# Optimization experiments

Hardware: AMD Instinct MI355X
Metric: run time of the kernel (lower is better)

Reference implementation:

```python
import jax, jax.numpy as jnp
import numpy as np

MARGIN = 0.1  # GatingFunction margin_threshold default


def _gating(x, gW1, gb1, gW2, gb2):
    # two-layer MLP + softmax over experts: [B, E]
    h = jax.nn.relu(x @ gW1 + gb1)
    probs = jax.nn.softmax(h @ gW2 + gb2, axis=1)

    # sequential per-sample running-assignment masking (training + mask_enabled path)
    def step(rta, s):
        rta1 = rta + s
        mask = rta1 > rta1.mean() + MARGIN
        rta2 = jnp.where(mask.any(), rta1 - s, rta1)  # subtract back only if any masked
        mod = jnp.where(mask, 0.0, s)
        norm = mod.sum()
        mod = mod / jnp.where(norm == 0, 1.0, norm)
        return rta2 + mod, mod

    rta0 = jnp.zeros((gW2.shape[1],), probs.dtype)  # running_total_assignment buffer
    _, gate = jax.lax.scan(step, rta0, probs)
    # torch code writes detached modified samples into modified_x -> no grad through gate
    return jax.lax.stop_gradient(gate)


def reference(x_expert, gW1, gb1, gW2, gb2, eW1, eb1, eW2, eb2):
    gate = _gating(x_expert, gW1, gb1, gW2, gb2)          # [B, E]
    # all experts run densely: [B, E, H] -> [B, E, O]
    h = jax.nn.relu(jnp.einsum('bi,eih->beh', x_expert, eW1) + eb1)
    expert_out = jnp.einsum('beh,eho->beo', h, eW2) + eb2
    g = gate[:, :, None]                                   # [B, E, 1]
    # fallback if every gate value is zero (torch's all-zero check)
    g = jnp.where(jnp.all(g == 0), jnp.ones_like(g) / g.shape[1], g)
    output = jnp.sum(g * expert_out, axis=1)               # [B, O]
    return output, g


def setup_inputs() -> dict:
    B, IN, HID, OUT, E = 4096, 1024, 4096, 1024, 8
    key = jax.random.key(0)
    ks = jax.random.split(key, 9)
    s = 0.02
    return {
        'x_expert': jax.random.normal(ks[0], (B, IN), jnp.float32),
        'gW1': jax.random.normal(ks[1], (IN, HID), jnp.float32) * s,
        'gb1': jnp.zeros((HID,), jnp.float32),
        'gW2': jax.random.normal(ks[2], (HID, E), jnp.float32) * s,
        'gb2': jnp.zeros((E,), jnp.float32),
        'eW1': jax.random.normal(ks[3], (E, IN, HID), jnp.float32) * s,
        'eb1': jnp.zeros((E, HID), jnp.float32),
        'eW2': jax.random.normal(ks[4], (E, HID, OUT), jnp.float32) * s,
        'eb2': jnp.zeros((E, OUT), jnp.float32),
    }
```

## Files before the change

### kernel.cpp

```cpp
#include <hip/hip_runtime.h>
#include <stdint.h>

using f32x4  = __attribute__((ext_vector_type(4))) float;
using bf16x8 = __attribute__((ext_vector_type(8))) __bf16;

static __device__ __forceinline__ unsigned int f2bf_u(float f) {
  union { float f; unsigned int u; } v; v.f = f;
  return (v.u + 0x7fffu + ((v.u >> 16) & 1u)) >> 16;
}
static __device__ __forceinline__ unsigned short f2bf(float f) {
  return (unsigned short)f2bf_u(f);
}

static __device__ __forceinline__ void gload_lds16(const void* g, void* l) {
  __builtin_amdgcn_global_load_lds((const __attribute__((address_space(1))) void*)g,
                                   (__attribute__((address_space(3))) void*)l,
                                   16, 0, 0);
}

static __device__ __forceinline__ int swz(int row) { return (row & 3) ^ ((row >> 2) & 3); }

template <int CTRL>
static __device__ __forceinline__ float dppadd(float x) {
  int xi = __builtin_bit_cast(int, x);
  int yi = __builtin_amdgcn_update_dpp(0, xi, CTRL, 0xF, 0xF, true);
  return x + __builtin_bit_cast(float, yi);
}
static __device__ __forceinline__ float redsum8(float x) {
  float t = dppadd<0xB1>(x);
  t = dppadd<0x4E>(t);
  t = dppadd<0x124>(t);
  return t;
}

__global__ __launch_bounds__(256) void k_cvt_bf16(const float* __restrict__ in,
                                                  unsigned short* __restrict__ out) {
  int i = blockIdx.x * 256 + threadIdx.x;
  float4 v = ((const float4*)in)[i];
  ushort4 o;
  o.x = f2bf(v.x); o.y = f2bf(v.y); o.z = f2bf(v.z); o.w = f2bf(v.w);
  ((ushort4*)out)[i] = o;
}

__global__ __launch_bounds__(256) void k_transpose_cvt(const float* __restrict__ in,
                                                       unsigned short* __restrict__ out,
                                                       int R, int C) {
  __shared__ float tile[32][33];
  int e = blockIdx.z;
  const float* ip = in + (size_t)e * R * C;
  unsigned short* op = out + (size_t)e * R * C;
  int c0 = blockIdx.x * 32, r0 = blockIdx.y * 32;
  int tx = threadIdx.x, ty = threadIdx.y;
  #pragma unroll
  for (int i = ty; i < 32; i += 8)
    tile[i][tx] = ip[(size_t)(r0 + i) * C + c0 + tx];
  __syncthreads();
  #pragma unroll
  for (int i = ty; i < 32; i += 8)
    op[(size_t)(c0 + i) * R + r0 + tx] = f2bf(tile[tx][i]);
}

__global__ __launch_bounds__(256, 2) void k_gemm_f32_relu(const float* __restrict__ A,
                                                          const float* __restrict__ Bm,
                                                          const float* __restrict__ bias,
                                                          float* __restrict__ C) {
  const int K = 1024, N = 4096;
  __shared__ float As[16][256];
  __shared__ float Bs[16][128];
  int n0 = blockIdx.x * 128, m0 = blockIdx.y * 256;
  int t = threadIdx.x;
  int tm = t >> 4, tn = t & 15;
  float acc[16][8];
  #pragma unroll
  for (int i = 0; i < 16; ++i)
    #pragma unroll
    for (int j = 0; j < 8; ++j) acc[i][j] = 0.f;

  for (int k0 = 0; k0 < K; k0 += 16) {
    __syncthreads();
    #pragma unroll
    for (int cc = 0; cc < 4; ++cc) {
      int c = t + cc * 256;
      int m = c >> 2, kq = c & 3;
      float4 v = *(const float4*)&A[(size_t)(m0 + m) * K + k0 + kq * 4];
      As[kq * 4 + 0][m] = v.x; As[kq * 4 + 1][m] = v.y;
      As[kq * 4 + 2][m] = v.z; As[kq * 4 + 3][m] = v.w;
    }
    #pragma unroll
    for (int cc = 0; cc < 2; ++cc) {
      int c = t + cc * 256;
      int kr = c >> 5, nq = c & 31;
      *(float4*)&Bs[kr][nq * 4] = *(const float4*)&Bm[(size_t)(k0 + kr) * N + n0 + nq * 4];
    }
    __syncthreads();
    #pragma unroll
    for (int kk = 0; kk < 16; ++kk) {
      float a[16], b[8];
      #pragma unroll
      for (int q = 0; q < 4; ++q)
        *(float4*)&a[q * 4] = *(const float4*)&As[kk][tm * 16 + q * 4];
      *(float4*)&b[0] = *(const float4*)&Bs[kk][tn * 8];
      *(float4*)&b[4] = *(const float4*)&Bs[kk][tn * 8 + 4];
      #pragma unroll
      for (int i = 0; i < 16; ++i)
        #pragma unroll
        for (int j = 0; j < 8; ++j) acc[i][j] = fmaf(a[i], b[j], acc[i][j]);
    }
  }
  float bb[8];
  #pragma unroll
  for (int j = 0; j < 8; ++j) bb[j] = bias[n0 + tn * 8 + j];
  #pragma unroll
  for (int i = 0; i < 16; ++i) {
    int m = m0 + tm * 16 + i;
    float* crow = C + (size_t)m * N + n0 + tn * 8;
    float4 v0, v1;
    v0.x = fmaxf(acc[i][0] + bb[0], 0.f); v0.y = fmaxf(acc[i][1] + bb[1], 0.f);
    v0.z = fmaxf(acc[i][2] + bb[2], 0.f); v0.w = fmaxf(acc[i][3] + bb[3], 0.f);
    v1.x = fmaxf(acc[i][4] + bb[4], 0.f); v1.y = fmaxf(acc[i][5] + bb[5], 0.f);
    v1.z = fmaxf(acc[i][6] + bb[6], 0.f); v1.w = fmaxf(acc[i][7] + bb[7], 0.f);
    *(float4*)crow = v0; *(float4*)(crow + 4) = v1;
  }
}

__global__ __launch_bounds__(256) void k_gate2_softmax(const float* __restrict__ Hg,
                                                       const float* __restrict__ gW2,
                                                       const float* __restrict__ gb2,
                                                       float* __restrict__ probs) {
  __shared__ float red[4][8];
  int b = blockIdx.x, t = threadIdx.x;
  const float* hrow = Hg + (size_t)b * 4096;
  float acc[8];
  #pragma unroll
  for (int e = 0; e < 8; ++e) acc[e] = 0.f;
  #pragma unroll
  for (int i = 0; i < 4; ++i) {
    int kk = t + i * 256;
    float4 h = ((const float4*)hrow)[kk];
    const float* wr = gW2 + (size_t)kk * 32;
    #pragma unroll
    for (int j = 0; j < 4; ++j) {
      float hv = (&h.x)[j];
      #pragma unroll
      for (int e = 0; e < 8; ++e) acc[e] = fmaf(hv, wr[j * 8 + e], acc[e]);
    }
  }
  #pragma unroll
  for (int e = 0; e < 8; ++e) {
    float v = acc[e];
    for (int off = 32; off > 0; off >>= 1) v += __shfl_down(v, off);
    acc[e] = v;
  }
  int lane = t & 63, w = t >> 6;
  if (lane == 0) {
    #pragma unroll
    for (int e = 0; e < 8; ++e) red[w][e] = acc[e];
  }
  __syncthreads();
  if (t == 0) {
    float l[8], mx = -1e30f;
    #pragma unroll
    for (int e = 0; e < 8; ++e) {
      l[e] = red[0][e] + red[1][e] + red[2][e] + red[3][e] + gb2[e];
      mx = fmaxf(mx, l[e]);
    }
    float sum = 0.f;
    #pragma unroll
    for (int e = 0; e < 8; ++e) { l[e] = expf(l[e] - mx); sum += l[e]; }
    float inv = 1.f / sum;
    #pragma unroll
    for (int e = 0; e < 8; ++e) probs[b * 8 + e] = l[e] * inv;
  }
}

__global__ __launch_bounds__(256) void k_egemm1_scan(const unsigned short* __restrict__ Xb,
                                                     const unsigned short* __restrict__ W1T,
                                                     const float* __restrict__ eb1,
                                                     const float* __restrict__ probs,
                                                     float* __restrict__ gateOut,
                                                     unsigned short* __restrict__ Hs) {
  __shared__ __align__(16) char smem[16512];
  int bid = blockIdx.x;
  int t = threadIdx.x;

  if (bid == 0) {
    float* P  = (float*)smem;
    float* G  = P + 2048;
    int*  flg = (int*)(G + 2048);
    int e = t & 7;
    float rta = 0.f, maxn = 0.f;
    for (int ch = 0; ch < 16; ++ch) {
      __syncthreads();
      #pragma unroll
      for (int i = 0; i < 2; ++i)
        ((float4*)P)[t + i * 256] = ((const float4*)(probs + ch * 2048))[t + i * 256];
      __syncthreads();
      if (t < 64) {
        float s_cur = P[e];
        for (int r = 0; r < 256; ++r) {
          float s_nxt = P[(((r + 1) & 255) << 3) + e];
          float a = rta + s_cur;
          float sum = redsum8(a);
          float thr = fmaf(sum, 0.125f, 0.1f);
          bool msk = a > thr;
          unsigned long long bal = __ballot(msk);
          float d = msk ? 0.f : s_cur;
          float norm = redsum8(d);
          float inv = (norm == 0.f) ? 1.f : (1.f / norm);
          float g = d * inv;
          float base = (bal != 0ull) ? (a - s_cur) : a;
          rta = base + g;
          maxn = fmaxf(maxn, norm);
          if (t < 8) G[(r << 3) + e] = g;
          s_cur = s_nxt;
        }
      }
      __syncthreads();
      #pragma unroll
      for (int i = 0; i < 2; ++i)
        ((float4*)(gateOut + ch * 2048))[t + i * 256] = ((const float4*)G)[t + i * 256];
    }
    if (t == 0) *flg = (maxn > 0.f) ? 1 : 0;
    __syncthreads();
    if (*flg == 0) {
      for (int i = t; i < 32768; i += 256) gateOut[i] = 0.125f;
    }
    return;
  }

  char* Asm = smem;
  char* Bsm = smem + 8192;
  int b = bid - 1;
  int e = b >> 10;
  int rest = b & 1023;
  int m0 = (rest >> 5) << 7, n0 = (rest & 31) << 7;
  int lane = t & 63, w = t >> 6;
  int wm = w >> 1, wn = w & 1;
  const unsigned short* Ab = Xb;
  const unsigned short* Bb = W1T + ((size_t)e << 22);
  f32x4 acc[4][4];
  #pragma unroll
  for (int mi = 0; mi < 4; ++mi)
    #pragma unroll
    for (int ni = 0; ni < 4; ++ni) acc[mi][ni] = (f32x4){0.f, 0.f, 0.f, 0.f};

  for (int kt = 0; kt < 1024; kt += 32) {
    __syncthreads();
    {
      int p = (w << 6) + lane;
      int row = p >> 2, h = (p & 3) ^ swz(row);
      int p2 = p + 256;
      int row2 = p2 >> 2, h2 = (p2 & 3) ^ swz(row2);
      char* la = Asm + (w << 10);
      char* lb = Bsm + (w << 10);
      gload_lds16(Ab + (size_t)(m0 + row) * 1024 + kt + h * 8, la);
      gload_lds16(Ab + (size_t)(m0 + row2) * 1024 + kt + h2 * 8, la + 4096);
      gload_lds16(Bb + (size_t)(n0 + row) * 1024 + kt + h * 8, lb);
      gload_lds16(Bb + (size_t)(n0 + row2) * 1024 + kt + h2 * 8, lb + 4096);
    }
    __syncthreads();
    bf16x8 af[4], bfr[4];
    #pragma unroll
    for (int mi = 0; mi < 4; ++mi) {
      int ra = (wm << 6) + (mi << 4) + (lane & 15);
      int hh = (lane >> 4) ^ swz(ra);
      af[mi] = *(const bf16x8*)(Asm + ra * 64 + hh * 16);
    }
    #pragma unroll
    for (int ni = 0; ni < 4; ++ni) {
      int rb = (wn << 6) + (ni << 4) + (lane & 15);
      int hh = (lane >> 4) ^ swz(rb);
      bfr[ni] = *(const bf16x8*)(Bsm + rb * 64 + hh * 16);
    }
    #pragma unroll
    for (int mi = 0; mi < 4; ++mi)
      #pragma unroll
      for (int ni = 0; ni < 4; ++ni)
        acc[mi][ni] = __builtin_amdgcn_mfma_f32_16x16x32_bf16(bfr[ni], af[mi], acc[mi][ni], 0, 0, 0);
  }
  const float* b1e = eb1 + (e << 12);
  unsigned short* Ho = Hs + ((size_t)e << 24);
  int col = lane & 15, quad = lane >> 4;
  float4 bq[4];
  #pragma unroll
  for (int ni = 0; ni < 4; ++ni)
    bq[ni] = *(const float4*)&b1e[n0 + (wn << 6) + (ni << 4) + (quad << 2)];
  #pragma unroll
  for (int mi = 0; mi < 4; ++mi) {
    int m = m0 + (wm << 6) + (mi << 4) + col;
    unsigned short* orow = Ho + (size_t)m * 4096 + n0 + (wn << 6) + (quad << 2);
    #pragma unroll
    for (int ni = 0; ni < 4; ++ni) {
      float v0 = fmaxf(acc[mi][ni][0] + bq[ni].x, 0.f);
      float v1 = fmaxf(acc[mi][ni][1] + bq[ni].y, 0.f);
      float v2 = fmaxf(acc[mi][ni][2] + bq[ni].z, 0.f);
      float v3 = fmaxf(acc[mi][ni][3] + bq[ni].w, 0.f);
      uint2 u;
      u.x = f2bf_u(v0) | (f2bf_u(v1) << 16);
      u.y = f2bf_u(v2) | (f2bf_u(v3) << 16);
      *(uint2*)(orow + (ni << 4)) = u;
    }
  }
}

__global__ __launch_bounds__(256) void k_egemm2(const unsigned short* __restrict__ Hs,
                                                const unsigned short* __restrict__ W2T,
                                                float* __restrict__ partLo,
                                                float* __restrict__ partHi) {
  __shared__ __align__(16) char Asm[8192];
  __shared__ __align__(16) char Bsm[8192];
  int bid = blockIdx.x;
  int n0 = (bid >> 8) << 7;
  int rem = bid & 255;
  int m0 = (rem >> 3) << 7;
  int e = rem & 7;
  int t = threadIdx.x, lane = t & 63, w = t >> 6;
  int wm = w >> 1, wn = w & 1;
  const unsigned short* Ab = Hs + ((size_t)e << 24);
  const unsigned short* Bb = W2T + ((size_t)e << 22);
  f32x4 acc[4][4];
  #pragma unroll
  for (int mi = 0; mi < 4; ++mi)
    #pragma unroll
    for (int ni = 0; ni < 4; ++ni) acc[mi][ni] = (f32x4){0.f, 0.f, 0.f, 0.f};

  for (int kt = 0; kt < 4096; kt += 32) {
    __syncthreads();
    {
      int p = (w << 6) + lane;
      int row = p >> 2, h = (p & 3) ^ swz(row);
      int p2 = p + 256;
      int row2 = p2 >> 2, h2 = (p2 & 3) ^ swz(row2);
      char* la = Asm + (w << 10);
      char* lb = Bsm + (w << 10);
      gload_lds16(Ab + (size_t)(m0 + row) * 4096 + kt + h * 8, la);
      gload_lds16(Ab + (size_t)(m0 + row2) * 4096 + kt + h2 * 8, la + 4096);
      gload_lds16(Bb + (size_t)(n0 + row) * 4096 + kt + h * 8, lb);
      gload_lds16(Bb + (size_t)(n0 + row2) * 4096 + kt + h2 * 8, lb + 4096);
    }
    __syncthreads();
    bf16x8 af[4], bfr[4];
    #pragma unroll
    for (int mi = 0; mi < 4; ++mi) {
      int ra = (wm << 6) + (mi << 4) + (lane & 15);
      int hh = (lane >> 4) ^ swz(ra);
      af[mi] = *(const bf16x8*)(Asm + ra * 64 + hh * 16);
    }
    #pragma unroll
    for (int ni = 0; ni < 4; ++ni) {
      int rb = (wn << 6) + (ni << 4) + (lane & 15);
      int hh = (lane >> 4) ^ swz(rb);
      bfr[ni] = *(const bf16x8*)(Bsm + rb * 64 + hh * 16);
    }
    #pragma unroll
    for (int mi = 0; mi < 4; ++mi)
      #pragma unroll
      for (int ni = 0; ni < 4; ++ni)
        acc[mi][ni] = __builtin_amdgcn_mfma_f32_16x16x32_bf16(bfr[ni], af[mi], acc[mi][ni], 0, 0, 0);
  }
  float* Pe = (e < 4 ? partLo + ((size_t)e << 22) : partHi + ((size_t)(e - 4) << 22));
  int col = lane & 15, quad = lane >> 4;
  #pragma unroll
  for (int mi = 0; mi < 4; ++mi) {
    int m = m0 + (wm << 6) + (mi << 4) + col;
    float* orow = Pe + (size_t)m * 1024 + n0 + (wn << 6) + (quad << 2);
    #pragma unroll
    for (int ni = 0; ni < 4; ++ni) {
      float4 v;
      v.x = acc[mi][ni][0]; v.y = acc[mi][ni][1];
      v.z = acc[mi][ni][2]; v.w = acc[mi][ni][3];
      *(float4*)(orow + (ni << 4)) = v;
    }
  }
}

__global__ __launch_bounds__(256) void k_reduce(const float* __restrict__ partLo,
                                                const float* __restrict__ partHi,
                                                const float* __restrict__ eb2,
                                                const float* __restrict__ gate,
                                                float* __restrict__ Out) {
  int idx = blockIdx.x * 256 + threadIdx.x;
  int m = idx >> 8, n4 = idx & 255;
  float4 g0 = *(const float4*)(gate + (m << 3));
  float4 g1 = *(const float4*)(gate + (m << 3) + 4);
  float ga[8] = {g0.x, g0.y, g0.z, g0.w, g1.x, g1.y, g1.z, g1.w};
  float4 acc = make_float4(0.f, 0.f, 0.f, 0.f);
  #pragma unroll
  for (int e = 0; e < 8; ++e) {
    const float* Pe = (e < 4 ? partLo + ((size_t)e << 22) : partHi + ((size_t)(e - 4) << 22));
    float4 pv = ((const float4*)Pe)[idx];
    float4 bv = ((const float4*)(eb2 + (e << 10)))[n4];
    acc.x += ga[e] * (pv.x + bv.x);
    acc.y += ga[e] * (pv.y + bv.y);
    acc.z += ga[e] * (pv.z + bv.z);
    acc.w += ga[e] * (pv.w + bv.w);
  }
  ((float4*)Out)[idx] = acc;
}

extern "C" void kernel_launch(void* const* d_in, const int* in_sizes, int n_in,
                              void* d_out, int out_size, void* d_ws, size_t ws_size,
                              hipStream_t stream) {
  (void)in_sizes; (void)n_in; (void)out_size; (void)ws_size;
  const float* x   = (const float*)d_in[0];
  const float* gW1 = (const float*)d_in[1];
  const float* gb1 = (const float*)d_in[2];
  const float* gW2 = (const float*)d_in[3];
  const float* gb2 = (const float*)d_in[4];
  const float* eW1 = (const float*)d_in[5];
  const float* eb1 = (const float*)d_in[6];
  const float* eW2 = (const float*)d_in[7];
  const float* eb2 = (const float*)d_in[8];
  float* out = (float*)d_out;
  float* gateOut = out + (size_t)4096 * 1024;

  char* ws = (char*)d_ws;
  unsigned short* Xb  = (unsigned short*)ws;
  unsigned short* W1T = (unsigned short*)(ws + (8ull  << 20));
  unsigned short* W2T = (unsigned short*)(ws + (72ull << 20));
  float*          prb = (float*)        (ws + (136ull << 20));
  float*          Hg  = (float*)        (ws + (137ull << 20));
  unsigned short* Hs  = (unsigned short*)(ws + (201ull << 20));
  float* partLo = (float*)(ws + (8ull   << 20));
  float* partHi = (float*)(ws + (137ull << 20));

  k_cvt_bf16<<<4096, 256, 0, stream>>>(x, Xb);
  k_transpose_cvt<<<dim3(128, 32, 8), dim3(32, 8), 0, stream>>>(eW1, W1T, 1024, 4096);
  k_transpose_cvt<<<dim3(32, 128, 8), dim3(32, 8), 0, stream>>>(eW2, W2T, 4096, 1024);
  k_gemm_f32_relu<<<dim3(32, 16), 256, 0, stream>>>(x, gW1, gb1, Hg);
  k_gate2_softmax<<<4096, 256, 0, stream>>>(Hg, gW2, gb2, prb);
  k_egemm1_scan<<<8193, 256, 0, stream>>>(Xb, W1T, eb1, prb, gateOut, Hs);
  k_egemm2<<<2048, 256, 0, stream>>>(Hs, W2T, partLo, partHi);
  k_reduce<<<4096, 256, 0, stream>>>(partLo, partHi, eb2, gateOut, out);
}
```

Before: 1.912 ms.

## Enlarge expert GEMM tiles to 256x256 with double-buffered LDS and grouped block order

Both expert GEMMs move from 128x128 tiles with 256 threads to 256x256 tiles with 512 threads. The LDS staging is now double-buffered, so the next K-slice loads while MFMAs run on the current one, and blocks are remapped into groups of eight for L2 locality. The scan block is adapted to 512 threads. This should raise arithmetic intensity and hide load latency, at the cost of more registers (32 accumulators per lane) and fewer blocks in flight, especially in egemm2 with only 512 blocks.

```diff
diff --git a/kernel.cpp b/kernel.cpp
--- a/kernel.cpp
+++ b/kernel.cpp
@@ -31,6 +31,21 @@
   t = dppadd<0x4E>(t);
   t = dppadd<0x124>(t);
   return t;
+}
+
+static __device__ __forceinline__ void stage_tiles(const unsigned short* __restrict__ gA,
+                                                   const unsigned short* __restrict__ gB,
+                                                   int strideK, int kt, int w, int lane,
+                                                   char* bufA, char* bufB) {
+  #pragma unroll
+  for (int r = 0; r < 2; ++r) {
+    int c = r * 512 + w * 64 + lane;
+    int row = c >> 2, h = (c & 3) ^ swz(row);
+    size_t go = (size_t)row * strideK + kt + h * 8;
+    int lo = (r * 512 + w * 64) << 4;
+    gload_lds16(gA + go, bufA + lo);
+    gload_lds16(gB + go, bufB + lo);
+  }
 }
 
 __global__ __launch_bounds__(256) void k_cvt_bf16(const float* __restrict__ in,
@@ -173,13 +188,13 @@
   }
 }
 
-__global__ __launch_bounds__(256) void k_egemm1_scan(const unsigned short* __restrict__ Xb,
-                                                     const unsigned short* __restrict__ W1T,
-                                                     const float* __restrict__ eb1,
-                                                     const float* __restrict__ probs,
-                                                     float* __restrict__ gateOut,
-                                                     unsigned short* __restrict__ Hs) {
-  __shared__ __align__(16) char smem[16512];
+__global__ __launch_bounds__(512, 2) void k_egemm1_scan(const unsigned short* __restrict__ Xb,
+                                                        const unsigned short* __restrict__ W1T,
+                                                        const float* __restrict__ eb1,
+                                                        const float* __restrict__ probs,
+                                                        float* __restrict__ gateOut,
+                                                        unsigned short* __restrict__ Hs) {
+  __shared__ __align__(16) char smem[65536];
   int bid = blockIdx.x;
   int t = threadIdx.x;
 
@@ -191,9 +206,7 @@
     float rta = 0.f, maxn = 0.f;
     for (int ch = 0; ch < 16; ++ch) {
       __syncthreads();
-      #pragma unroll
-      for (int i = 0; i < 2; ++i)
-        ((float4*)P)[t + i * 256] = ((const float4*)(probs + ch * 2048))[t + i * 256];
+      ((float4*)P)[t] = ((const float4*)(probs + ch * 2048))[t];
       __syncthreads();
       if (t < 64) {
         float s_cur = P[e];
@@ -216,67 +229,61 @@
         }
       }
       __syncthreads();
-      #pragma unroll
-      for (int i = 0; i < 2; ++i)
-        ((float4*)(gateOut + ch * 2048))[t + i * 256] = ((const float4*)G)[t + i * 256];
+      ((float4*)(gateOut + ch * 2048))[t] = ((const float4*)G)[t];
     }
     if (t == 0) *flg = (maxn > 0.f) ? 1 : 0;
     __syncthreads();
     if (*flg == 0) {
-      for (int i = t; i < 32768; i += 256) gateOut[i] = 0.125f;
+      for (int i = t; i < 32768; i += 512) gateOut[i] = 0.125f;
     }
     return;
   }
 
-  char* Asm = smem;
-  char* Bsm = smem + 8192;
   int b = bid - 1;
-  int e = b >> 10;
-  int rest = b & 1023;
-  int m0 = (rest >> 5) << 7, n0 = (rest & 31) << 7;
+  int G8 = b >> 7, within = b & 127;
+  int m = within >> 3, x = within & 7;
+  int g = G8 * 8 + x;
+  int e = g >> 4, n = g & 15;
+  int m0 = m << 8, n0 = n << 8;
   int lane = t & 63, w = t >> 6;
-  int wm = w >> 1, wn = w & 1;
-  const unsigned short* Ab = Xb;
-  const unsigned short* Bb = W1T + ((size_t)e << 22);
-  f32x4 acc[4][4];
-  #pragma unroll
-  for (int mi = 0; mi < 4; ++mi)
+  int wm = w >> 2, wn = w & 3;
+  const unsigned short* Ag = Xb + (size_t)m0 * 1024;
+  const unsigned short* Bg = W1T + ((size_t)e << 22) + (size_t)n0 * 1024;
+  f32x4 acc[8][4];
+  #pragma unroll
+  for (int mi = 0; mi < 8; ++mi)
     #pragma unroll
     for (int ni = 0; ni < 4; ++ni) acc[mi][ni] = (f32x4){0.f, 0.f, 0.f, 0.f};
 
+  stage_tiles(Ag, Bg, 1024, 0, w, lane, smem, smem + 16384);
+  __syncthreads();
   for (int kt = 0; kt < 1024; kt += 32) {
-    __syncthreads();
-    {
-      int p = (w << 6) + lane;
-      int row = p >> 2, h = (p & 3) ^ swz(row);
-      int p2 = p + 256;
-      int row2 = p2 >> 2, h2 = (p2 & 3) ^ swz(row2);
-      char* la = Asm + (w << 10);
-      char* lb = Bsm + (w << 10);
-      gload_lds16(Ab + (size_t)(m0 + row) * 1024 + kt + h * 8, la);
-      gload_lds16(Ab + (size_t)(m0 + row2) * 1024 + kt + h2 * 8, la + 4096);
-      gload_lds16(Bb + (size_t)(n0 + row) * 1024 + kt + h * 8, lb);
-      gload_lds16(Bb + (size_t)(n0 + row2) * 1024 + kt + h2 * 8, lb + 4096);
-    }
-    __syncthreads();
-    bf16x8 af[4], bfr[4];
-    #pragma unroll
-    for (int mi = 0; mi < 4; ++mi) {
-      int ra = (wm << 6) + (mi << 4) + (lane & 15);
+    int cur = (kt >> 5) & 1;
+    char* cA = smem + (cur << 15);
+    char* cB = cA + 16384;
+    if (kt + 32 < 1024) {
+      char* nA = smem + ((cur ^ 1) << 15);
+      stage_tiles(Ag, Bg, 1024, kt + 32, w, lane, nA, nA + 16384);
+    }
+    bf16x8 af[8], bfr[4];
+    #pragma unroll
+    for (int mi = 0; mi < 8; ++mi) {
+      int ra = (wm << 7) + (mi << 4) + (lane & 15);
       int hh = (lane >> 4) ^ swz(ra);
-      af[mi] = *(const bf16x8*)(Asm + ra * 64 + hh * 16);
+      af[mi] = *(const bf16x8*)(cA + ra * 64 + hh * 16);
     }
     #pragma unroll
     for (int ni = 0; ni < 4; ++ni) {
       int rb = (wn << 6) + (ni << 4) + (lane & 15);
       int hh = (lane >> 4) ^ swz(rb);
-      bfr[ni] = *(const bf16x8*)(Bsm + rb * 64 + hh * 16);
-    }
-    #pragma unroll
-    for (int mi = 0; mi < 4; ++mi)
+      bfr[ni] = *(const bf16x8*)(cB + rb * 64 + hh * 16);
+    }
+    #pragma unroll
+    for (int mi = 0; mi < 8; ++mi)
       #pragma unroll
       for (int ni = 0; ni < 4; ++ni)
         acc[mi][ni] = __builtin_amdgcn_mfma_f32_16x16x32_bf16(bfr[ni], af[mi], acc[mi][ni], 0, 0, 0);
+    __syncthreads();
   }
   const float* b1e = eb1 + (e << 12);
   unsigned short* Ho = Hs + ((size_t)e << 24);
@@ -286,9 +293,9 @@
   for (int ni = 0; ni < 4; ++ni)
     bq[ni] = *(const float4*)&b1e[n0 + (wn << 6) + (ni << 4) + (quad << 2)];
   #pragma unroll
-  for (int mi = 0; mi < 4; ++mi) {
-    int m = m0 + (wm << 6) + (mi << 4) + col;
-    unsigned short* orow = Ho + (size_t)m * 4096 + n0 + (wn << 6) + (quad << 2);
+  for (int mi = 0; mi < 8; ++mi) {
+    int mm = m0 + (wm << 7) + (mi << 4) + col;
+    unsigned short* orow = Ho + (size_t)mm * 4096 + n0 + (wn << 6) + (quad << 2);
     #pragma unroll
     for (int ni = 0; ni < 4; ++ni) {
       float v0 = fmaxf(acc[mi][ni][0] + bq[ni].x, 0.f);
@@ -303,67 +310,63 @@
   }
 }
 
-__global__ __launch_bounds__(256) void k_egemm2(const unsigned short* __restrict__ Hs,
-                                                const unsigned short* __restrict__ W2T,
-                                                float* __restrict__ partLo,
-                                                float* __restrict__ partHi) {
-  __shared__ __align__(16) char Asm[8192];
-  __shared__ __align__(16) char Bsm[8192];
+__global__ __launch_bounds__(512, 2) void k_egemm2(const unsigned short* __restrict__ Hs,
+                                                   const unsigned short* __restrict__ W2T,
+                                                   float* __restrict__ partLo,
+                                                   float* __restrict__ partHi) {
+  __shared__ __align__(16) char smem[65536];
   int bid = blockIdx.x;
-  int n0 = (bid >> 8) << 7;
-  int rem = bid & 255;
-  int m0 = (rem >> 3) << 7;
-  int e = rem & 7;
+  int G8 = bid >> 5, within = bid & 31;
+  int n = within >> 3, x = within & 7;
+  int g = G8 * 8 + x;
+  int e = g >> 4, m = g & 15;
+  int m0 = m << 8, n0 = n << 8;
   int t = threadIdx.x, lane = t & 63, w = t >> 6;
-  int wm = w >> 1, wn = w & 1;
-  const unsigned short* Ab = Hs + ((size_t)e << 24);
-  const unsigned short* Bb = W2T + ((size_t)e << 22);
-  f32x4 acc[4][4];
-  #pragma unroll
-  for (int mi = 0; mi < 4; ++mi)
+  int wm = w >> 2, wn = w & 3;
+  const unsigned short* Ag = Hs + ((size_t)e << 24) + (size_t)m0 * 4096;
+  const unsigned short* Bg = W2T + ((size_t)e << 22) + (size_t)n0 * 4096;
+  f32x4 acc[8][4];
+  #pragma unroll
+  for (int mi = 0; mi < 8; ++mi)
     #pragma unroll
     for (int ni = 0; ni < 4; ++ni) acc[mi][ni] = (f32x4){0.f, 0.f, 0.f, 0.f};
 
+  stage_tiles(Ag, Bg, 4096, 0, w, lane, smem, smem + 16384);
+  __syncthreads();
   for (int kt = 0; kt < 4096; kt += 32) {
-    __syncthreads();
-    {
-      int p = (w << 6) + lane;
-      int row = p >> 2, h = (p & 3) ^ swz(row);
-      int p2 = p + 256;
-      int row2 = p2 >> 2, h2 = (p2 & 3) ^ swz(row2);
-      char* la = Asm + (w << 10);
-      char* lb = Bsm + (w << 10);
-      gload_lds16(Ab + (size_t)(m0 + row) * 4096 + kt + h * 8, la);
-      gload_lds16(Ab + (size_t)(m0 + row2) * 4096 + kt + h2 * 8, la + 4096);
-      gload_lds16(Bb + (size_t)(n0 + row) * 4096 + kt + h * 8, lb);
-      gload_lds16(Bb + (size_t)(n0 + row2) * 4096 + kt + h2 * 8, lb + 4096);
-    }
-    __syncthreads();
-    bf16x8 af[4], bfr[4];
-    #pragma unroll
-    for (int mi = 0; mi < 4; ++mi) {
-      int ra = (wm << 6) + (mi << 4) + (lane & 15);
+    int cur = (kt >> 5) & 1;
+    char* cA = smem + (cur << 15);
+    char* cB = cA + 16384;
+    if (kt + 32 < 4096) {
+      char* nA = smem + ((cur ^ 1) << 15);
+      stage_tiles(Ag, Bg, 4096, kt + 32, w, lane, nA, nA + 16384);
+    }
+    bf16x8 af[8], bfr[4];
+    #pragma unroll
+    for (int mi = 0; mi < 8; ++mi) {
+      int ra = (wm << 7) + (mi << 4) + (lane & 15);
       int hh = (lane >> 4) ^ swz(ra);
-      af[mi] = *(const bf16x8*)(Asm + ra * 64 + hh * 16);
+      af[mi] = *(const bf16x8*)(cA + ra * 64 + hh * 16);
     }
     #pragma unroll
     for (int ni = 0; ni < 4; ++ni) {
       int rb = (wn << 6) + (ni << 4) + (lane & 15);
       int hh = (lane >> 4) ^ swz(rb);
-      bfr[ni] = *(const bf16x8*)(Bsm + rb * 64 + hh * 16);
-    }
-    #pragma unroll
-    for (int mi = 0; mi < 4; ++mi)
+      bfr[ni] = *(const bf16x8*)(cB + rb * 64 + hh * 16);
+    }
+    #pragma unroll
+    for (int mi = 0; mi < 8; ++mi)
       #pragma unroll
       for (int ni = 0; ni < 4; ++ni)
         acc[mi][ni] = __builtin_amdgcn_mfma_f32_16x16x32_bf16(bfr[ni], af[mi], acc[mi][ni], 0, 0, 0);
+    __syncthreads();
   }
   float* Pe = (e < 4 ? partLo + ((size_t)e << 22) : partHi + ((size_t)(e - 4) << 22));
   int col = lane & 15, quad = lane >> 4;
   #pragma unroll
-  for (int mi = 0; mi < 4; ++mi) {
-    int m = m0 + (wm << 6) + (mi << 4) + col;
-    float* orow = Pe + (size_t)m * 1024 + n0 + (wn << 6) + (quad << 2);
+  for (int mi = 0; mi < 8; ++mi) {
+    int mm = m0 + (wm << 7) + (mi << 4) + col;
+    float* orow = Pe + (size_t)mm * 1024 + n0 + (wn << 6) + (quad << 2);
     #pragma unroll
     for (int ni = 0; ni < 4; ++ni) {
       float4 v;
@@ -429,7 +432,7 @@
   k_transpose_cvt<<<dim3(32, 128, 8), dim3(32, 8), 0, stream>>>(eW2, W2T, 4096, 1024);
   k_gemm_f32_relu<<<dim3(32, 16), 256, 0, stream>>>(x, gW1, gb1, Hg);
   k_gate2_softmax<<<4096, 256, 0, stream>>>(Hg, gW2, gb2, prb);
-  k_egemm1_scan<<<8193, 256, 0, stream>>>(Xb, W1T, eb1, prb, gateOut, Hs);
-  k_egemm2<<<2048, 256, 0, stream>>>(Hs, W2T, partLo, partHi);
+  k_egemm1_scan<<<2049, 512, 0, stream>>>(Xb, W1T, eb1, prb, gateOut, Hs);
+  k_egemm2<<<512, 512, 0, stream>>>(Hs, W2T, partLo, partHi);
   k_reduce<<<4096, 256, 0, stream>>>(partLo, partHi, eb2, gateOut, out);
 }
```

After: 1.656 ms. -13.4%, faster.
